# Kernel optimization log

Measured on AMD Instinct MI355X. Metric: run time of the kernel, lower is better.

Reference implementation:

```python
import jax, jax.numpy as jnp
import numpy as np

NUM_LEVELS = 4
RADIUS = 4


def _bilinear_sample(vol, x, y):
    """grid_sample(align_corners=True, padding_mode='zeros') at pixel coords.
    vol: [N, H, W]; x, y: [N, P] float pixel coordinates. Returns [N, P]."""
    N, H, W = vol.shape
    x0 = jnp.floor(x)
    y0 = jnp.floor(y)
    x1 = x0 + 1.0
    y1 = y0 + 1.0
    wx1 = x - x0
    wx0 = 1.0 - wx1
    wy1 = y - y0
    wy0 = 1.0 - wy1
    flat = vol.reshape(N, H * W)

    def gather(yc, xc):
        valid = (xc >= 0) & (xc <= W - 1) & (yc >= 0) & (yc <= H - 1)
        xi = jnp.clip(xc, 0, W - 1).astype(jnp.int32)
        yi = jnp.clip(yc, 0, H - 1).astype(jnp.int32)
        v = jnp.take_along_axis(flat, yi * W + xi, axis=1)
        return jnp.where(valid, v, jnp.zeros((), vol.dtype))

    return (gather(y0, x0) * wy0 * wx0 + gather(y0, x1) * wy0 * wx1 +
            gather(y1, x0) * wy1 * wx0 + gather(y1, x1) * wy1 * wx1)


def setup_inputs() -> dict:
    key = jax.random.key(0)
    k1, k2, k3 = jax.random.split(key, 3)
    bs, dim, h, w = 1, 256, 64, 128
    fmap1 = jax.random.normal(k1, (bs, dim, h, w), dtype=jnp.float32)
    fmap2 = jax.random.normal(k2, (bs, dim, h, w), dtype=jnp.float32)
    # pixel-coordinate grid (x, y) + flow-like perturbation, as RAFT's coords1
    xs = jnp.arange(w, dtype=jnp.float32)
    ys = jnp.arange(h, dtype=jnp.float32)
    gy, gx = jnp.meshgrid(ys, xs, indexing='ij')
    base = jnp.stack([gx, gy], axis=0)[None]  # [1, 2, h, w]
    coords = base + 4.0 * jax.random.normal(k3, (bs, 2, h, w), dtype=jnp.float32)
    return {"fmap1": fmap1, "fmap2": fmap2, "coords": coords}


def reference(fmap1, fmap2, coords):
    bs, dim, h, w = fmap1.shape
    f1 = fmap1.reshape(bs, dim, h * w)
    f2 = fmap2.reshape(bs, dim, h * w)
    # all-pairs cost volume: [bs, h*w, h*w], scaled by 1/sqrt(dim)
    cv = jnp.einsum('bcm,bcn->bmn', f1, f2) / jnp.sqrt(
        jnp.asarray(dim, fmap1.dtype))
    cv = cv.reshape(bs * h * w, h, w)
    pyramid = [cv]
    for _ in range(NUM_LEVELS - 1):
        N, H, W = cv.shape
        cv = cv.reshape(N, H // 2, 2, W // 2, 2).mean(axis=(2, 4))  # avg_pool2d(2,2)
        pyramid.append(cv)

    c = coords.transpose(0, 2, 3, 1).reshape(bs * h * w, 2)  # (x, y) per pixel
    r = RADIUS
    d = jnp.linspace(-r, r, 2 * r + 1, dtype=coords.dtype)
    # torch code: delta = stack(meshgrid(dy, dx, 'ij'), -1); delta[...,0] is
    # added to x, delta[...,1] to y (kept identical for channel-order fidelity)
    dyg, dxg = jnp.meshgrid(d, d, indexing='ij')
    off_x = dyg.reshape(-1)[None, :]  # [1, 81]
    off_y = dxg.reshape(-1)[None, :]

    outs = []
    for i in range(NUM_LEVELS):
        scale = jnp.asarray(2 ** i, coords.dtype)
        x_s = c[:, :1] / scale + off_x  # [bs*h*w, 81]
        y_s = c[:, 1:] / scale + off_y
        corr = _bilinear_sample(pyramid[i], x_s, y_s)
        outs.append(corr.reshape(bs, h, w, -1))
    out = jnp.concatenate(outs, axis=-1)          # [bs, h, w, 4*81]
    return out.transpose(0, 3, 1, 2)              # [bs, 324, h, w]
```

## Files before the change

### kernel.cpp

```cpp
#include <hip/hip_runtime.h>
#include <hip/hip_bf16.h>

#define HW   8192
#define W0   128
#define H0   64
#define CDIM 256

typedef int int4v __attribute__((ext_vector_type(4)));

__device__ __forceinline__ int4v mfma_i8_16x16x64(int4v a, int4v b, int4v c) {
    asm volatile("v_mfma_i32_16x16x64_i8 %0, %1, %2, %0"
                 : "+v"(c) : "v"(a), "v"(b));
    return c;
}

__global__ __launch_bounds__(256) void k_q_f1(const float* __restrict__ in,
                                              signed char* __restrict__ q1,
                                              float* __restrict__ s1) {
    __shared__ float lds[32][257];
    __shared__ float sInv[32];
    __shared__ float sSc[32];
    const int m0 = blockIdx.x * 32;
    const int tc = threadIdx.x & 31;
    const int tr = threadIdx.x >> 5;
    #pragma unroll 4
    for (int r = 0; r < 32; ++r) {
        const int c = r * 8 + tr;
        lds[tc][c] = in[(size_t)c * HW + m0 + tc];
    }
    __syncthreads();
    const int row = threadIdx.x >> 3, t8 = threadIdx.x & 7;
    float am = 0.f;
    #pragma unroll 8
    for (int k = 0; k < 32; ++k) am = fmaxf(am, fabsf(lds[row][t8 * 32 + k]));
    am = fmaxf(am, __shfl_xor(am, 1));
    am = fmaxf(am, __shfl_xor(am, 2));
    am = fmaxf(am, __shfl_xor(am, 4));
    if (t8 == 0) {
        sInv[row] = am > 0.f ? 127.f / am : 0.f;
        sSc[row]  = (am / 127.f) * 0.0625f;
    }
    __syncthreads();
    const int c = threadIdx.x;
    #pragma unroll 4
    for (int ml = 0; ml < 32; ++ml) {
        q1[(size_t)(m0 + ml) * CDIM + c] =
            (signed char)__float2int_rn(lds[ml][c] * sInv[ml]);
    }
    if (threadIdx.x < 32) s1[m0 + threadIdx.x] = sSc[threadIdx.x];
}

__global__ __launch_bounds__(256) void k_transpose_f2(const float* __restrict__ in,
                                                      _Float16* __restrict__ outT) {
    __shared__ float lds[32][257];
    const int m0 = blockIdx.x * 32;
    const int tc = threadIdx.x & 31;
    const int tr = threadIdx.x >> 5;
    #pragma unroll 4
    for (int r = 0; r < 32; ++r) {
        const int c = r * 8 + tr;
        lds[tc][c] = in[(size_t)c * HW + m0 + tc];
    }
    __syncthreads();
    const int c = threadIdx.x;
    #pragma unroll 4
    for (int ml = 0; ml < 32; ++ml) {
        outT[(size_t)(m0 + ml) * CDIM + c] = (_Float16)lds[ml][c];
    }
}

__global__ __launch_bounds__(256) void k_pool(const _Float16* __restrict__ in,
                                              _Float16* __restrict__ out,
                                              int Wout, int Win) {
    const int c = threadIdx.x;
    const int b = blockIdx.x;
    const int X = b % Wout;
    const int Y = b / Wout;
    const size_t base = ((size_t)(2 * Y) * Win + 2 * X) * CDIM + c;
    const size_t rows = (size_t)Win * CDIM;
    float s = (float)in[base] + (float)in[base + CDIM] +
              (float)in[base + rows] + (float)in[base + rows + CDIM];
    out[(size_t)b * CDIM + c] = (_Float16)(s * 0.25f);
}

__global__ __launch_bounds__(256) void k_quant(const _Float16* __restrict__ pf,
                                               unsigned int* __restrict__ pq,
                                               float* __restrict__ s2, int ntex) {
    const int t = blockIdx.x * 4 + (threadIdx.x >> 6);
    if (t >= ntex) return;
    const int lane = threadIdx.x & 63;
    const _Float16* p = pf + (size_t)t * CDIM + lane * 4;
    const float a0 = (float)p[0], a1 = (float)p[1], a2 = (float)p[2], a3 = (float)p[3];
    float am = fmaxf(fmaxf(fabsf(a0), fabsf(a1)), fmaxf(fabsf(a2), fabsf(a3)));
    #pragma unroll
    for (int d = 1; d < 64; d <<= 1) am = fmaxf(am, __shfl_xor(am, d));
    const float inv = am > 0.f ? 127.f / am : 0.f;
    const unsigned int q0 = (unsigned int)__float2int_rn(a0 * inv) & 255u;
    const unsigned int q1 = (unsigned int)__float2int_rn(a1 * inv) & 255u;
    const unsigned int q2 = (unsigned int)__float2int_rn(a2 * inv) & 255u;
    const unsigned int q3 = (unsigned int)__float2int_rn(a3 * inv) & 255u;
    pq[(size_t)t * 64 + lane] = q0 | (q1 << 8) | (q2 << 16) | (q3 << 24);
    if (lane == 0) s2[t] = am / 127.f;
}

__global__ __launch_bounds__(1024, 4) void k_sample_mfma(
        const signed char* __restrict__ q1, const float* __restrict__ s1,
        const unsigned char* __restrict__ pyrQ, const float* __restrict__ s2,
        const float* __restrict__ coords, float* __restrict__ out) {
    const int tid  = threadIdx.x;
    const int wv   = tid >> 6;
    const int lane = tid & 63;
    const int m0   = blockIdx.x * 16;

    __shared__ float sG[16][4][105];
    __shared__ float sF[16][4][2];
    __shared__ float sS[16];
    __shared__ int   sX0[4][16];
    __shared__ int   sY0[4][16];

    {
        float* gz = &sG[0][0][0];
        for (int k = tid; k < 16 * 4 * 105; k += 1024) gz[k] = 0.f;
    }
    if (tid < 16) {
        sS[tid] = s1[m0 + tid];
        const float cx = coords[m0 + tid];
        const float cy = coords[HW + m0 + tid];
        #pragma unroll
        for (int w = 0; w < 4; ++w) {
            const float scale = 1.0f / (float)(1 << w);
            const float xs = cx * scale, ys = cy * scale;
            const float X0f = floorf(xs), Y0f = floorf(ys);
            sX0[w][tid] = (int)X0f;
            sY0[w][tid] = (int)Y0f;
            sF[tid][w][0] = xs - X0f;
            sF[tid][w][1] = ys - Y0f;
        }
    }
    __syncthreads();

    const signed char* ap = q1 + (size_t)(m0 + (lane & 15)) * CDIM + ((lane >> 4) << 4);
    const int4v A0 = *reinterpret_cast<const int4v*>(ap);
    const int4v A1 = *reinterpret_cast<const int4v*>(ap + 64);
    const int4v A2 = *reinterpret_cast<const int4v*>(ap + 128);
    const int4v A3 = *reinterpret_cast<const int4v*>(ap + 192);

    #pragma unroll
    for (int w = 0; w < 4; ++w) {
        const int Wl = W0 >> w;
        const int Hl = H0 >> w;
        const int texoff = (w == 0) ? 0 : (w == 1) ? 8192 : (w == 2) ? 10240 : 10752;
        const signed char* lvl = (const signed char*)pyrQ + ((size_t)texoff << 8);
        const float* s2l = s2 + texoff;

        int minX = 1 << 30, maxX = -(1 << 30), minY = 1 << 30, maxY = -(1 << 30);
        #pragma unroll
        for (int p = 0; p < 16; ++p) {
            const int x0 = sX0[w][p], y0 = sY0[w][p];
            minX = min(minX, x0); maxX = max(maxX, x0);
            minY = min(minY, y0); maxY = max(maxY, y0);
        }
        const int xlo = max(minX - 4, 0), xhi = min(maxX + 5, Wl - 1);
        const int ylo = max(minY - 4, 0), yhi = min(maxY + 5, Hl - 1);
        if (xlo > xhi || ylo > yhi) continue;
        const int span  = xhi - xlo + 1;
        const int cpr   = (span + 15) >> 4;
        const int items = (yhi - ylo + 1) * cpr;

        for (int it = wv; it < items; it += 16) {
            const int rowi = it / cpr;
            const int gy   = ylo + rowi;
            const int t0   = xlo + (it - rowi * cpr) * 16;
            const int gxl  = t0 + (lane & 15);
            const int gxc  = min(gxl, xhi);
            const signed char* bp = lvl + (((size_t)(gy * Wl + gxc)) << 8) + ((lane >> 4) << 4);
            int4v acc = {0, 0, 0, 0};
            acc = mfma_i8_16x16x64(A0, *reinterpret_cast<const int4v*>(bp),       acc);
            acc = mfma_i8_16x16x64(A1, *reinterpret_cast<const int4v*>(bp + 64),  acc);
            acc = mfma_i8_16x16x64(A2, *reinterpret_cast<const int4v*>(bp + 128), acc);
            acc = mfma_i8_16x16x64(A3, *reinterpret_cast<const int4v*>(bp + 192), acc);
            const float s2v = s2l[gy * Wl + gxc];
            const bool xok = (gxl <= xhi);
            #pragma unroll
            for (int r = 0; r < 4; ++r) {
                const int px = ((lane >> 4) << 2) + r;
                const int j = gy - sY0[w][px] + 4;
                const int i = gxl - sX0[w][px] + 4;
                if (xok && (unsigned)j < 10u && (unsigned)i < 10u)
                    sG[px][w][j * 10 + i] = (float)acc[r] * s2v;
            }
        }
    }
    __syncthreads();

    const int cpx = tid & 15;
    const float s1v = sS[cpx];
    for (int o = tid >> 4; o < 324; o += 64) {
        const int lev = (o * 811) >> 16;
        const int k   = o - lev * 81;
        const int a   = (k * 57) >> 9;
        const int bb  = k - a * 9;
        const float fx = sF[cpx][lev][0], fy = sF[cpx][lev][1];
        const float wx0 = 1.0f - fx, wy0 = 1.0f - fy;
        const float* G = sG[cpx][lev];
        const float v = wy0 * (wx0 * G[bb * 10 + a]       + fx * G[bb * 10 + a + 1])
                      + fy  * (wx0 * G[(bb + 1) * 10 + a] + fx * G[(bb + 1) * 10 + a + 1]);
        out[(size_t)o * HW + m0 + cpx] = v * s1v;
    }
}

extern "C" void kernel_launch(void* const* d_in, const int* in_sizes, int n_in,
                              void* d_out, int out_size, void* d_ws, size_t ws_size,
                              hipStream_t stream) {
    const float* fmap1  = (const float*)d_in[0];
    const float* fmap2  = (const float*)d_in[1];
    const float* coords = (const float*)d_in[2];
    float* out = (float*)d_out;

    char* ws = (char*)d_ws;
    signed char* q1  = (signed char*)ws;
    float* s1        = (float*)(ws + 2097152);
    float* s2        = (float*)(ws + 2129920);
    unsigned char* pyrQ = (unsigned char*)(ws + 2176000);
    _Float16* pyrF   = (_Float16*)(ws + 4961280);
    _Float16* p0 = pyrF;
    _Float16* p1 = pyrF + 2097152;
    _Float16* p2 = pyrF + 2621440;
    _Float16* p3 = pyrF + 2752512;

    k_transpose_f2<<<HW / 32, 256, 0, stream>>>(fmap2, p0);
    k_pool<<<32 * 64, 256, 0, stream>>>(p0, p1, 64, 128);
    k_pool<<<16 * 32, 256, 0, stream>>>(p1, p2, 32, 64);
    k_pool<<<8 * 16, 256, 0, stream>>>(p2, p3, 16, 32);
    k_quant<<<(10880 + 3) / 4, 256, 0, stream>>>(pyrF, (unsigned int*)pyrQ, s2, 10880);
    k_q_f1<<<HW / 32, 256, 0, stream>>>(fmap1, q1, s1);
    k_sample_mfma<<<HW / 16, 1024, 0, stream>>>(q1, s1, pyrQ, s2, coords, out);
}
```

Measured before the change: 62.98 us.

## Fuse fmap2 prep into two kernels and widen sampler to 32 pixels

Merges transpose, the three pooling passes and quantization of fmap2 into two kernels. The first transposes and quantizes level 0. The second pools levels 1-3 straight from level 0 and quantizes them, which removes three launches and the intermediate fp16 pyramid traffic. The sampling kernel now handles 32 query pixels per block, so each B tile load is shared by two MFMA chains. It also replaces the integer division in the tile loop with a magic-number multiply. In exchange, each block does more window work over a larger bounding box, uses more LDS, and the grid has fewer blocks.

```diff
diff --git a/kernel.cpp b/kernel.cpp
--- a/kernel.cpp
+++ b/kernel.cpp
@@ -50,9 +50,13 @@
     if (threadIdx.x < 32) s1[m0 + threadIdx.x] = sSc[threadIdx.x];
 }
 
-__global__ __launch_bounds__(256) void k_transpose_f2(const float* __restrict__ in,
-                                                      _Float16* __restrict__ outT) {
+__global__ __launch_bounds__(256) void k_tq_f2(const float* __restrict__ in,
+                                               _Float16* __restrict__ p0,
+                                               signed char* __restrict__ q0,
+                                               float* __restrict__ s2) {
     __shared__ float lds[32][257];
+    __shared__ float sInv[32];
+    __shared__ float sSc[32];
     const int m0 = blockIdx.x * 32;
     const int tc = threadIdx.x & 31;
     const int tr = threadIdx.x >> 5;
@@ -62,67 +66,83 @@
         lds[tc][c] = in[(size_t)c * HW + m0 + tc];
     }
     __syncthreads();
+    const int row = threadIdx.x >> 3, t8 = threadIdx.x & 7;
+    float am = 0.f;
+    #pragma unroll 8
+    for (int k = 0; k < 32; ++k) am = fmaxf(am, fabsf(lds[row][t8 * 32 + k]));
+    am = fmaxf(am, __shfl_xor(am, 1));
+    am = fmaxf(am, __shfl_xor(am, 2));
+    am = fmaxf(am, __shfl_xor(am, 4));
+    if (t8 == 0) {
+        sInv[row] = am > 0.f ? 127.f / am : 0.f;
+        sSc[row]  = am / 127.f;
+    }
+    __syncthreads();
     const int c = threadIdx.x;
     #pragma unroll 4
     for (int ml = 0; ml < 32; ++ml) {
-        outT[(size_t)(m0 + ml) * CDIM + c] = (_Float16)lds[ml][c];
-    }
-}
-
-__global__ __launch_bounds__(256) void k_pool(const _Float16* __restrict__ in,
-                                              _Float16* __restrict__ out,
-                                              int Wout, int Win) {
-    const int c = threadIdx.x;
+        const float v = lds[ml][c];
+        p0[(size_t)(m0 + ml) * CDIM + c] = (_Float16)v;
+        q0[(size_t)(m0 + ml) * CDIM + c] = (signed char)__float2int_rn(v * sInv[ml]);
+    }
+    if (threadIdx.x < 32) s2[m0 + threadIdx.x] = sSc[threadIdx.x];
+}
+
+__global__ __launch_bounds__(256) void k_pq(const _Float16* __restrict__ p0,
+                                            signed char* __restrict__ pyrQ,
+                                            float* __restrict__ s2) {
     const int b = blockIdx.x;
-    const int X = b % Wout;
-    const int Y = b / Wout;
-    const size_t base = ((size_t)(2 * Y) * Win + 2 * X) * CDIM + c;
-    const size_t rows = (size_t)Win * CDIM;
-    float s = (float)in[base] + (float)in[base + CDIM] +
-              (float)in[base + rows] + (float)in[base + rows + CDIM];
-    out[(size_t)b * CDIM + c] = (_Float16)(s * 0.25f);
-}
-
-__global__ __launch_bounds__(256) void k_quant(const _Float16* __restrict__ pf,
-                                               unsigned int* __restrict__ pq,
-                                               float* __restrict__ s2, int ntex) {
-    const int t = blockIdx.x * 4 + (threadIdx.x >> 6);
-    if (t >= ntex) return;
-    const int lane = threadIdx.x & 63;
-    const _Float16* p = pf + (size_t)t * CDIM + lane * 4;
-    const float a0 = (float)p[0], a1 = (float)p[1], a2 = (float)p[2], a3 = (float)p[3];
-    float am = fmaxf(fmaxf(fabsf(a0), fabsf(a1)), fmaxf(fabsf(a2), fabsf(a3)));
+    int w, t;
+    if (b < 2048)      { w = 1; t = b; }
+    else if (b < 2560) { w = 2; t = b - 2048; }
+    else               { w = 3; t = b - 2560; }
+    const int Wl = W0 >> w;
+    const int f  = 1 << w;
+    const int X  = t & (Wl - 1);
+    const int Y  = t / Wl;
+    const int c  = threadIdx.x;
+
+    float s = 0.f;
+    for (int dy = 0; dy < f; ++dy) {
+        const size_t rb = ((size_t)(Y * f + dy) * W0 + X * f) * CDIM + c;
+        for (int dx = 0; dx < f; ++dx) s += (float)p0[rb + (size_t)dx * CDIM];
+    }
+    const float v = s / (float)(f * f);
+
+    __shared__ float wmax[4];
+    float am = fabsf(v);
     #pragma unroll
     for (int d = 1; d < 64; d <<= 1) am = fmaxf(am, __shfl_xor(am, d));
+    if ((threadIdx.x & 63) == 0) wmax[threadIdx.x >> 6] = am;
+    __syncthreads();
+    am = fmaxf(fmaxf(wmax[0], wmax[1]), fmaxf(wmax[2], wmax[3]));
     const float inv = am > 0.f ? 127.f / am : 0.f;
-    const unsigned int q0 = (unsigned int)__float2int_rn(a0 * inv) & 255u;
-    const unsigned int q1 = (unsigned int)__float2int_rn(a1 * inv) & 255u;
-    const unsigned int q2 = (unsigned int)__float2int_rn(a2 * inv) & 255u;
-    const unsigned int q3 = (unsigned int)__float2int_rn(a3 * inv) & 255u;
-    pq[(size_t)t * 64 + lane] = q0 | (q1 << 8) | (q2 << 16) | (q3 << 24);
-    if (lane == 0) s2[t] = am / 127.f;
+
+    const int texoff = (w == 1) ? 8192 : (w == 2) ? 10240 : 10752;
+    pyrQ[((size_t)(texoff + t) << 8) + c] = (signed char)__float2int_rn(v * inv);
+    if (threadIdx.x == 0) s2[texoff + t] = am / 127.f;
 }
 
 __global__ __launch_bounds__(1024, 4) void k_sample_mfma(
         const signed char* __restrict__ q1, const float* __restrict__ s1,
-        const unsigned char* __restrict__ pyrQ, const float* __restrict__ s2,
+        const signed char* __restrict__ pyrQ, const float* __restrict__ s2,
         const float* __restrict__ coords, float* __restrict__ out) {
     const int tid  = threadIdx.x;
     const int wv   = tid >> 6;
     const int lane = tid & 63;
-    const int m0   = blockIdx.x * 16;
-
-    __shared__ float sG[16][4][105];
-    __shared__ float sF[16][4][2];
-    __shared__ float sS[16];
-    __shared__ int   sX0[4][16];
-    __shared__ int   sY0[4][16];
+    const int m0   = blockIdx.x * 32;
+
+    __shared__ float sG[32][4][105];
+    __shared__ float sF[32][4][2];
+    __shared__ float sS[32];
+    __shared__ int   sX0[4][32];
+    __shared__ int   sY0[4][32];
 
     {
         float* gz = &sG[0][0][0];
-        for (int k = tid; k < 16 * 4 * 105; k += 1024) gz[k] = 0.f;
-    }
-    if (tid < 16) {
+        for (int k = tid; k < 32 * 4 * 105; k += 1024) gz[k] = 0.f;
+    }
+    if (tid < 32) {
         sS[tid] = s1[m0 + tid];
         const float cx = coords[m0 + tid];
         const float cy = coords[HW + m0 + tid];
@@ -139,23 +159,28 @@
     }
     __syncthreads();
 
-    const signed char* ap = q1 + (size_t)(m0 + (lane & 15)) * CDIM + ((lane >> 4) << 4);
-    const int4v A0 = *reinterpret_cast<const int4v*>(ap);
-    const int4v A1 = *reinterpret_cast<const int4v*>(ap + 64);
-    const int4v A2 = *reinterpret_cast<const int4v*>(ap + 128);
-    const int4v A3 = *reinterpret_cast<const int4v*>(ap + 192);
+    const signed char* ap0 = q1 + (size_t)(m0 + (lane & 15)) * CDIM + ((lane >> 4) << 4);
+    const signed char* ap1 = ap0 + 16 * CDIM;
+    const int4v A0 = *reinterpret_cast<const int4v*>(ap0);
+    const int4v A1 = *reinterpret_cast<const int4v*>(ap0 + 64);
+    const int4v A2 = *reinterpret_cast<const int4v*>(ap0 + 128);
+    const int4v A3 = *reinterpret_cast<const int4v*>(ap0 + 192);
+    const int4v A4 = *reinterpret_cast<const int4v*>(ap1);
+    const int4v A5 = *reinterpret_cast<const int4v*>(ap1 + 64);
+    const int4v A6 = *reinterpret_cast<const int4v*>(ap1 + 128);
+    const int4v A7 = *reinterpret_cast<const int4v*>(ap1 + 192);
 
     #pragma unroll
     for (int w = 0; w < 4; ++w) {
         const int Wl = W0 >> w;
         const int Hl = H0 >> w;
         const int texoff = (w == 0) ? 0 : (w == 1) ? 8192 : (w == 2) ? 10240 : 10752;
-        const signed char* lvl = (const signed char*)pyrQ + ((size_t)texoff << 8);
+        const signed char* lvl = pyrQ + ((size_t)texoff << 8);
         const float* s2l = s2 + texoff;
 
         int minX = 1 << 30, maxX = -(1 << 30), minY = 1 << 30, maxY = -(1 << 30);
         #pragma unroll
-        for (int p = 0; p < 16; ++p) {
+        for (int p = 0; p < 32; ++p) {
             const int x0 = sX0[w][p], y0 = sY0[w][p];
             minX = min(minX, x0); maxX = max(maxX, x0);
             minY = min(minY, y0); maxY = max(maxY, y0);
@@ -166,36 +191,55 @@
         const int span  = xhi - xlo + 1;
         const int cpr   = (span + 15) >> 4;
         const int items = (yhi - ylo + 1) * cpr;
+        const unsigned mgc = (16777215u / (unsigned)cpr) + 1u;
 
         for (int it = wv; it < items; it += 16) {
-            const int rowi = it / cpr;
+            const int rowi = (int)(((unsigned long long)(unsigned)it * mgc) >> 24);
             const int gy   = ylo + rowi;
             const int t0   = xlo + (it - rowi * cpr) * 16;
             const int gxl  = t0 + (lane & 15);
             const int gxc  = min(gxl, xhi);
             const signed char* bp = lvl + (((size_t)(gy * Wl + gxc)) << 8) + ((lane >> 4) << 4);
-            int4v acc = {0, 0, 0, 0};
-            acc = mfma_i8_16x16x64(A0, *reinterpret_cast<const int4v*>(bp),       acc);
-            acc = mfma_i8_16x16x64(A1, *reinterpret_cast<const int4v*>(bp + 64),  acc);
-            acc = mfma_i8_16x16x64(A2, *reinterpret_cast<const int4v*>(bp + 128), acc);
-            acc = mfma_i8_16x16x64(A3, *reinterpret_cast<const int4v*>(bp + 192), acc);
+            const int4v B0 = *reinterpret_cast<const int4v*>(bp);
+            const int4v B1 = *reinterpret_cast<const int4v*>(bp + 64);
+            const int4v B2 = *reinterpret_cast<const int4v*>(bp + 128);
+            const int4v B3 = *reinterpret_cast<const int4v*>(bp + 192);
+            int4v acc0 = {0, 0, 0, 0};
+            int4v acc1 = {0, 0, 0, 0};
+            acc0 = mfma_i8_16x16x64(A0, B0, acc0);
+            acc1 = mfma_i8_16x16x64(A4, B0, acc1);
+            acc0 = mfma_i8_16x16x64(A1, B1, acc0);
+            acc1 = mfma_i8_16x16x64(A5, B1, acc1);
+            acc0 = mfma_i8_16x16x64(A2, B2, acc0);
+            acc1 = mfma_i8_16x16x64(A6, B2, acc1);
+            acc0 = mfma_i8_16x16x64(A3, B3, acc0);
+            acc1 = mfma_i8_16x16x64(A7, B3, acc1);
             const float s2v = s2l[gy * Wl + gxc];
             const bool xok = (gxl <= xhi);
             #pragma unroll
             for (int r = 0; r < 4; ++r) {
                 const int px = ((lane >> 4) << 2) + r;
-                const int j = gy - sY0[w][px] + 4;
-                const int i = gxl - sX0[w][px] + 4;
-                if (xok && (unsigned)j < 10u && (unsigned)i < 10u)
-                    sG[px][w][j * 10 + i] = (float)acc[r] * s2v;
+                {
+                    const int j = gy - sY0[w][px] + 4;
+                    const int i = gxl - sX0[w][px] + 4;
+                    if (xok && (unsigned)j < 10u && (unsigned)i < 10u)
+                        sG[px][w][j * 10 + i] = (float)acc0[r] * s2v;
+                }
+                {
+                    const int px1 = px + 16;
+                    const int j = gy - sY0[w][px1] + 4;
+                    const int i = gxl - sX0[w][px1] + 4;
+                    if (xok && (unsigned)j < 10u && (unsigned)i < 10u)
+                        sG[px1][w][j * 10 + i] = (float)acc1[r] * s2v;
+                }
             }
         }
     }
     __syncthreads();
 
-    const int cpx = tid & 15;
+    const int cpx = tid & 31;
     const float s1v = sS[cpx];
-    for (int o = tid >> 4; o < 324; o += 64) {
+    for (int o = tid >> 5; o < 324; o += 32) {
         const int lev = (o * 811) >> 16;
         const int k   = o - lev * 81;
         const int a   = (k * 57) >> 9;
@@ -221,18 +265,11 @@
     signed char* q1  = (signed char*)ws;
     float* s1        = (float*)(ws + 2097152);
     float* s2        = (float*)(ws + 2129920);
-    unsigned char* pyrQ = (unsigned char*)(ws + 2176000);
-    _Float16* pyrF   = (_Float16*)(ws + 4961280);
-    _Float16* p0 = pyrF;
-    _Float16* p1 = pyrF + 2097152;
-    _Float16* p2 = pyrF + 2621440;
-    _Float16* p3 = pyrF + 2752512;
-
-    k_transpose_f2<<<HW / 32, 256, 0, stream>>>(fmap2, p0);
-    k_pool<<<32 * 64, 256, 0, stream>>>(p0, p1, 64, 128);
-    k_pool<<<16 * 32, 256, 0, stream>>>(p1, p2, 32, 64);
-    k_pool<<<8 * 16, 256, 0, stream>>>(p2, p3, 16, 32);
-    k_quant<<<(10880 + 3) / 4, 256, 0, stream>>>(pyrF, (unsigned int*)pyrQ, s2, 10880);
+    signed char* pyrQ = (signed char*)(ws + 2176000);
+    _Float16* p0     = (_Float16*)(ws + 4961280);
+
+    k_tq_f2<<<HW / 32, 256, 0, stream>>>(fmap2, p0, pyrQ, s2);
+    k_pq<<<2688, 256, 0, stream>>>(p0, pyrQ, s2);
     k_q_f1<<<HW / 32, 256, 0, stream>>>(fmap1, q1, s1);
-    k_sample_mfma<<<HW / 16, 1024, 0, stream>>>(q1, s1, pyrQ, s2, coords, out);
-}
+    k_sample_mfma<<<HW / 32, 1024, 0, stream>>>(q1, s1, pyrQ, s2, coords, out);
+}
```

Measured after the change: 74.02 us. 17.5% more time.
